# Performance work log

Hardware: AMD Instinct MI355X
Metric: run time of the kernel (lower is better)

The kernel has to match this reference:

```python
import jax, jax.numpy as jnp
import numpy as np

DIM = 64
B_GRAPHS = 16
N_NODES = 4096
N_EDGES = 16384
SLOPE = 0.01  # PyTorch leaky_relu default negative slope


def lrelu(x):
    return jnp.where(x >= 0, x, SLOPE * x)


def setup_inputs() -> dict:
    key = jax.random.key(0)
    ks = jax.random.split(key, 16)
    d = DIM

    def rn(k, shape, scale=0.05):
        return jax.random.normal(k, shape, dtype=jnp.float32) * scale

    def z(*s):
        return jnp.zeros(s, jnp.float32)

    return {
        "x": jax.random.normal(ks[0], (N_NODES, 3), dtype=jnp.float32),
        "edge_attr": jax.random.normal(ks[1], (N_EDGES, 4), dtype=jnp.float32),
        "edge_index": jax.random.randint(ks[2], (2, N_EDGES), 0, N_NODES),
        "batch": jnp.sort(jax.random.randint(ks[3], (N_NODES,), 0, B_GRAPHS)),
        # lin0
        "W0": rn(ks[4], (3, d)), "b0": z(d),
        # edge MLP: Linear(4,d) -> LeakyReLU -> Linear(d, d*d)
        "We1": rn(ks[5], (4, d)), "be1": z(d),
        "We2": rn(ks[6], (d, d * d), 0.01), "be2": z(d * d),
        # NNConv root weight + bias
        "root": rn(ks[7], (d, d)), "conv_b": z(d),
        # GRU(d, d)  (PyTorch layout: [3d, in] / [3d, hid], gate order r,z,n)
        "Wih": rn(ks[8], (3 * d, d)), "Whh": rn(ks[9], (3 * d, d)),
        "bih": z(3 * d), "bhh": z(3 * d),
        # Set2Set LSTM(2d, d)  (gate order i,f,g,o)
        "lWih": rn(ks[10], (4 * d, 2 * d)), "lWhh": rn(ks[11], (4 * d, d)),
        "lbih": z(4 * d), "lbhh": z(4 * d),
        # lin_out: Linear(2d, 2)
        "Wout": rn(ks[12], (2 * d, 2)), "bout": z(2),
    }


def _forward(x, edge_attr, W0, b0, We1, be1, We2, be2, root, conv_b,
             Wih, Whh, bih, bhh, lWih, lWhh, lbih, lbhh, Wout, bout,
             edge_index, batch):
    d = DIM
    N = x.shape[0]
    E = edge_attr.shape[0]
    src, dst = edge_index[0], edge_index[1]  # messages flow src(j) -> dst(i)

    out = lrelu(x @ W0 + b0)  # [N, d]
    h = out                    # GRU hidden state (h = out.unsqueeze(0))

    # Edge-conditioned weights: constant across the 6 iterations, compute once.
    he = lrelu(edge_attr @ We1 + be1)          # [E, d]
    W_e = (he @ We2 + be2).reshape(E, d, d)    # [E, d, d]
    deg = jax.ops.segment_sum(jnp.ones((E,), jnp.float32), dst, num_segments=N)
    inv_deg = (1.0 / jnp.maximum(deg, 1.0))[:, None]  # mean aggr, clamp like PyG

    for _ in range(6):
        # NNConv: gather x_j, per-edge matmul, scatter-mean, plus root term
        msg = jnp.einsum('ed,edf->ef', out[src], W_e)            # [E, d]
        agg = jax.ops.segment_sum(msg, dst, num_segments=N) * inv_deg
        m = lrelu(agg + out @ root + conv_b)                     # [N, d]
        # GRU cell (single step, PyTorch gate order r, z, n)
        gi = m @ Wih.T + bih
        gh = h @ Whh.T + bhh
        i_r, i_z, i_n = jnp.split(gi, 3, axis=-1)
        h_r, h_z, h_n = jnp.split(gh, 3, axis=-1)
        r = jax.nn.sigmoid(i_r + h_r)
        zg = jax.nn.sigmoid(i_z + h_z)
        n = jnp.tanh(i_n + r * h_n)
        h = (1.0 - zg) * n + zg * h
        out = h

    # Set2Set pooling, processing_steps = 1
    Bg = B_GRAPHS
    q_star = jnp.zeros((Bg, 2 * d), jnp.float32)
    hl = jnp.zeros((Bg, d), jnp.float32)
    cl = jnp.zeros((Bg, d), jnp.float32)
    gates = q_star @ lWih.T + lbih + hl @ lWhh.T + lbhh
    gi_, gf_, gg_, go_ = jnp.split(gates, 4, axis=-1)
    cl = jax.nn.sigmoid(gf_) * cl + jax.nn.sigmoid(gi_) * jnp.tanh(gg_)
    q = jax.nn.sigmoid(go_) * jnp.tanh(cl)         # [Bg, d]
    e = jnp.sum(out * q[batch], axis=-1)           # [N]
    emax = jax.ops.segment_max(e, batch, num_segments=Bg)
    a = jnp.exp(e - emax[batch])
    asum = jax.ops.segment_sum(a, batch, num_segments=Bg)
    a = a / asum[batch]                            # per-graph softmax attention
    rpool = jax.ops.segment_sum(a[:, None] * out, batch, num_segments=Bg)
    q_star = jnp.concatenate([q, rpool], axis=-1)  # [Bg, 2d]

    return q_star @ Wout + bout                    # [Bg, 2]


def reference(x, edge_attr, edge_index, batch, W0, b0, We1, be1, We2, be2,
              root, conv_b, Wih, Whh, bih, bhh, lWih, lWhh, lbih, lbhh,
              Wout, bout):
    return _forward(x, edge_attr, W0, b0, We1, be1, We2, be2, root, conv_b,
                    Wih, Whh, bih, bhh, lWih, lWhh, lbih, lbhh, Wout, bout,
                    edge_index, batch)
```

## Files before the change

kernel.cpp:

```cpp
#include <hip/hip_runtime.h>
#include <cstddef>

#define NE 16384
#define NN 4096
#define BG 16
#define NT 16
#define ACH 16

__device__ __forceinline__ float lrelu(float v){ return v >= 0.f ? v : 0.01f*v; }
__device__ __forceinline__ float sigm(float v){ return 1.f/(1.f + expf(-v)); }

__global__ __launch_bounds__(256) void setup_kernel(
    const float* __restrict__ x, const float* __restrict__ ea,
    const int* __restrict__ ei,
    const float* __restrict__ W0, const float* __restrict__ b0,
    const float* __restrict__ We1, const float* __restrict__ be1,
    const float* __restrict__ Wih, const float* __restrict__ Whh,
    float* __restrict__ WihT, float* __restrict__ WhhT,
    float* __restrict__ h, float* __restrict__ he,
    int* __restrict__ deg, int* __restrict__ cnt)
{
    int t = blockIdx.x*256 + threadIdx.x;
    {
        int e = t >> 6, f = t & 63;
        float v = be1[f];
        #pragma unroll
        for (int d = 0; d < 4; ++d) v += ea[e*4+d]*We1[d*64+f];
        he[t] = lrelu(v);
    }
    if (t < NN*64) {
        int n = t >> 6, f = t & 63;
        float v = b0[f];
        #pragma unroll
        for (int d = 0; d < 3; ++d) v += x[n*3+d]*W0[d*64+f];
        h[t] = lrelu(v);
    }
    if (t < 12288) {
        int k = t / 192, g = t - k*192;
        WihT[t] = Wih[g*64 + k];
        WhhT[t] = Whh[g*64 + k];
    }
    if (t < NE) {
        atomicAdd(&deg[ei[NE + t]], 1);
        atomicAdd(&cnt[ei[t]], 1);
    }
}

__global__ __launch_bounds__(256) void scan_kernel(const int* __restrict__ cnt,
                                                   int* __restrict__ offs)
{
    __shared__ int ps[256];
    int t = threadIdx.x;
    int base = t*16;
    int loc[16];
    int s = 0;
    #pragma unroll
    for (int i = 0; i < 16; ++i) { loc[i] = s; s += cnt[base+i]; }
    ps[t] = s; __syncthreads();
    for (int off = 1; off < 256; off <<= 1) {
        int v = 0;
        if (t >= off) v = ps[t-off];
        __syncthreads();
        if (t >= off) ps[t] += v;
        __syncthreads();
    }
    int pre = (t == 0) ? 0 : ps[t-1];
    #pragma unroll
    for (int i = 0; i < 16; ++i) offs[base+i] = pre + loc[i];
    if (t == 255) offs[NN] = pre + s;
}

__global__ __launch_bounds__(256) void scatter_kernel(
    const int* __restrict__ ei, const int* __restrict__ offs,
    int* __restrict__ cnt,
    int* __restrict__ srcs, int* __restrict__ dsts, int* __restrict__ perm)
{
    int e = blockIdx.x*256 + threadIdx.x;
    if (e >= NE) return;
    int s = ei[e], d = ei[NE + e];
    int old = atomicSub(&cnt[s], 1);
    int pos = offs[s] + old - 1;
    srcs[pos] = s; dsts[pos] = d; perm[pos] = e;
}

__global__ __launch_bounds__(256) void reorder_kernel(
    const float* __restrict__ he, const int* __restrict__ perm,
    float* __restrict__ he_srt)
{
    int t = blockIdx.x*256 + threadIdx.x;
    he_srt[t] = he[(size_t)perm[t>>6]*64 + (t & 63)];
}

__global__ __launch_bounds__(256) void inv_range_kernel(
    const int* __restrict__ deg, const int* __restrict__ batch,
    float* __restrict__ inv_deg, int* __restrict__ gstart, int* __restrict__ gend)
{
    int n = blockIdx.x*256 + threadIdx.x;
    if (n >= NN) return;
    inv_deg[n] = 1.f / fmaxf((float)deg[n], 1.f);
    int b  = batch[n];
    int bp = (n == 0)    ? -1 : batch[n-1];
    int bn = (n == NN-1) ? BG : batch[n+1];
    for (int g = bp+1; g <= b; ++g) gstart[g] = n;
    for (int g = b;   g <  bn; ++g) gend[g]   = n+1;
    if (n == 0)    for (int g = 0;   g < b;  ++g) gend[g]   = 0;
    if (n == NN-1) for (int g = b+1; g < BG; ++g) gstart[g] = NN;
}

__global__ __launch_bounds__(1024) void conv_kernel(
    const float* __restrict__ h, const float* __restrict__ We2,
    const float* __restrict__ be2, const float* __restrict__ he_srt,
    const int* __restrict__ offs, const int* __restrict__ srcs,
    const int* __restrict__ dsts, float* __restrict__ agg)
{
    __shared__ float hsT[64][NT];
    __shared__ float Tb [NT][64];
    __shared__ float Tc [ACH][NT][64];
    int t  = threadIdx.x;
    int n0 = blockIdx.x * NT;

    {
        int n = t >> 6, i = t & 63;
        hsT[i][n] = h[(size_t)(n0+n)*64 + i];
    }
    __syncthreads();
    {
        int n = t >> 6, f = t & 63;
        float acc = 0.f;
        #pragma unroll 8
        for (int i = 0; i < 64; ++i) acc += hsT[i][n] * be2[i*64+f];
        Tb[n][f] = acc;
    }

    int ebase = offs[n0];
    int ecnt  = offs[n0+NT] - ebase;
    int eend  = ebase + ecnt;
    int slot  = t >> 4;
    int f4    = (t & 15) * 4;
    int e0 = ebase + slot, e1 = ebase + slot + 64;
    int nl0 = -1, dt0 = 0, nl1 = -1, dt1 = 0;
    if (slot < ecnt)       { nl0 = srcs[e0] - n0; dt0 = dsts[e0]; }
    if (slot + 64 < ecnt)  { nl1 = srcs[e1] - n0; dt1 = dsts[e1]; }
    float4 m0 = {0,0,0,0}, m1 = {0,0,0,0};

    int aT = t >> 6;
    int fT = (t & 15) * 4;
    int nT = ((t >> 4) & 3) * 4;

    for (int c = 0; c < 4; ++c) {
        const float* Wp = We2 + ((size_t)(c*ACH + aT))*4096 + fT;
        float4 A0 = {0,0,0,0}, A1 = {0,0,0,0}, A2 = {0,0,0,0}, A3 = {0,0,0,0};
        #pragma unroll 8
        for (int i = 0; i < 64; ++i) {
            float4 w  = *(const float4*)(Wp + (size_t)i*64);
            float4 hv = *(const float4*)&hsT[i][nT];
            A0.x += hv.x*w.x; A0.y += hv.x*w.y; A0.z += hv.x*w.z; A0.w += hv.x*w.w;
            A1.x += hv.y*w.x; A1.y += hv.y*w.y; A1.z += hv.y*w.z; A1.w += hv.y*w.w;
            A2.x += hv.z*w.x; A2.y += hv.z*w.y; A2.z += hv.z*w.z; A2.w += hv.z*w.w;
            A3.x += hv.w*w.x; A3.y += hv.w*w.y; A3.z += hv.w*w.z; A3.w += hv.w*w.w;
        }
        __syncthreads();
        *(float4*)&Tc[aT][nT+0][fT] = A0;
        *(float4*)&Tc[aT][nT+1][fT] = A1;
        *(float4*)&Tc[aT][nT+2][fT] = A2;
        *(float4*)&Tc[aT][nT+3][fT] = A3;
        __syncthreads();

        if (nl0 >= 0) {
            const float* hep = he_srt + (size_t)e0*64 + c*ACH;
            #pragma unroll
            for (int a = 0; a < ACH; ++a) {
                float hv = hep[a];
                float4 tv = *(const float4*)&Tc[a][nl0][f4];
                m0.x += hv*tv.x; m0.y += hv*tv.y; m0.z += hv*tv.z; m0.w += hv*tv.w;
            }
        }
        if (nl1 >= 0) {
            const float* hep = he_srt + (size_t)e1*64 + c*ACH;
            #pragma unroll
            for (int a = 0; a < ACH; ++a) {
                float hv = hep[a];
                float4 tv = *(const float4*)&Tc[a][nl1][f4];
                m1.x += hv*tv.x; m1.y += hv*tv.y; m1.z += hv*tv.z; m1.w += hv*tv.w;
            }
        }
        for (int e = ebase + 128 + slot; e < eend; e += 64) {
            int nl = srcs[e] - n0, dt = dsts[e];
            const float* hep = he_srt + (size_t)e*64 + c*ACH;
            float4 pm = {0,0,0,0};
            #pragma unroll
            for (int a = 0; a < ACH; ++a) {
                float hv = hep[a];
                float4 tv = *(const float4*)&Tc[a][nl][f4];
                pm.x += hv*tv.x; pm.y += hv*tv.y; pm.z += hv*tv.z; pm.w += hv*tv.w;
            }
            if (c == 0) {
                float4 b = *(const float4*)&Tb[nl][f4];
                pm.x += b.x; pm.y += b.y; pm.z += b.z; pm.w += b.w;
            }
            float* ap = agg + (size_t)dt*64 + f4;
            atomicAdd(ap+0, pm.x); atomicAdd(ap+1, pm.y);
            atomicAdd(ap+2, pm.z); atomicAdd(ap+3, pm.w);
        }
    }

    if (nl0 >= 0) {
        float4 b = *(const float4*)&Tb[nl0][f4];
        float* ap = agg + (size_t)dt0*64 + f4;
        atomicAdd(ap+0, m0.x+b.x); atomicAdd(ap+1, m0.y+b.y);
        atomicAdd(ap+2, m0.z+b.z); atomicAdd(ap+3, m0.w+b.w);
    }
    if (nl1 >= 0) {
        float4 b = *(const float4*)&Tb[nl1][f4];
        float* ap = agg + (size_t)dt1*64 + f4;
        atomicAdd(ap+0, m1.x+b.x); atomicAdd(ap+1, m1.y+b.y);
        atomicAdd(ap+2, m1.z+b.z); atomicAdd(ap+3, m1.w+b.w);
    }
}

__global__ __launch_bounds__(512) void node_kernel(
    const float* __restrict__ WihT, const float* __restrict__ WhhT,
    const float* __restrict__ root, const float* __restrict__ conv_b,
    const float* __restrict__ inv_deg, const float* __restrict__ bih,
    const float* __restrict__ bhh, float* __restrict__ h,
    float* __restrict__ agg)
{
    __shared__ float WT[64][392];
    __shared__ float hT[64][34];
    __shared__ float mT[64][34];
    int t  = threadIdx.x;
    int n0 = blockIdx.x * 32;

    #pragma unroll
    for (int i = 0; i < 24; ++i) {
        int idx = t + i*512;
        int k = idx / 192, c = idx - k*192;
        WT[k][c]       = WihT[idx];
        WT[k][196 + c] = WhhT[idx];
    }
    #pragma unroll
    for (int i = 0; i < 4; ++i) {
        int idx = t + i*512;
        int n = idx >> 6, d = idx & 63;
        hT[d][n] = h[(size_t)(n0+n)*64 + d];
    }
    __syncthreads();
    #pragma unroll
    for (int i = 0; i < 4; ++i) {
        int idx = t + i*512;
        int n = idx >> 6, d = idx & 63;
        int gn = n0 + n;
        float v = agg[(size_t)gn*64 + d]*inv_deg[gn] + conv_b[d];
        agg[(size_t)gn*64 + d] = 0.f;
        #pragma unroll 8
        for (int k = 0; k < 64; ++k) v += hT[k][n]*root[k*64 + d];
        mT[d][n] = lrelu(v);
    }
    __syncthreads();

    int tx = t & 31, ty = t >> 5;
    float ai[2][2][3] = {{{0.f}}};
    float ah[2][2][3] = {{{0.f}}};
    #pragma unroll 8
    for (int k = 0; k < 64; ++k) {
        float2 am = *(float2*)&mT[k][ty*2];
        float2 av = *(float2*)&hT[k][ty*2];
        #pragma unroll
        for (int g = 0; g < 3; ++g) {
            float2 bi = *(float2*)&WT[k][g*64 + tx*2];
            float2 bh = *(float2*)&WT[k][196 + g*64 + tx*2];
            ai[0][0][g] += am.x*bi.x; ai[0][1][g] += am.x*bi.y;
            ai[1][0][g] += am.y*bi.x; ai[1][1][g] += am.y*bi.y;
            ah[0][0][g] += av.x*bh.x; ah[0][1][g] += av.x*bh.y;
            ah[1][0][g] += av.y*bh.x; ah[1][1][g] += av.y*bh.y;
        }
    }
    #pragma unroll
    for (int i = 0; i < 2; ++i) {
        int n = ty*2 + i, gn = n0 + n;
        #pragma unroll
        for (int j = 0; j < 2; ++j) {
            int g = tx*2 + j;
            float r  = sigm(ai[i][j][0] + bih[g]      + ah[i][j][0] + bhh[g]);
            float z  = sigm(ai[i][j][1] + bih[64+g]   + ah[i][j][1] + bhh[64+g]);
            float nn = tanhf(ai[i][j][2] + bih[128+g] + r*(ah[i][j][2] + bhh[128+g]));
            float ho = hT[g][n];
            h[(size_t)gn*64 + g] = (1.f - z)*nn + z*ho;
        }
    }
}

__device__ __forceinline__ float q_val(const float* lbih, const float* lbhh, int g)
{
    float gi = lbih[g]     + lbhh[g];
    float gg = lbih[128+g] + lbhh[128+g];
    float go = lbih[192+g] + lbhh[192+g];
    return sigm(go)*tanhf(sigm(gi)*tanhf(gg));
}

__global__ __launch_bounds__(256) void e_kernel(
    const float* __restrict__ h, const float* __restrict__ lbih,
    const float* __restrict__ lbhh, float* __restrict__ e)
{
    __shared__ float qs[64];
    int t = threadIdx.x;
    if (t < 64) qs[t] = q_val(lbih, lbhh, t);
    __syncthreads();
    int w = t >> 6, f = t & 63;
    int n = blockIdx.x*4 + w;
    float p = h[(size_t)n*64 + f]*qs[f];
    #pragma unroll
    for (int off = 32; off; off >>= 1) p += __shfl_xor(p, off);
    if (f == 0) e[n] = p;
}

__global__ __launch_bounds__(1024) void pool_kernel(
    const float* __restrict__ h, float* __restrict__ e,
    const int* __restrict__ gstart, const int* __restrict__ gend,
    const float* __restrict__ lbih, const float* __restrict__ lbhh,
    const float* __restrict__ Wout, const float* __restrict__ bout,
    float* __restrict__ out)
{
    __shared__ float red[1024];
    __shared__ float rp[64];
    __shared__ float sval;
    int g = blockIdx.x, t = threadIdx.x;
    int s = gstart[g], en = gend[g];

    float mx = -1e30f;
    for (int n = s+t; n < en; n += 1024) mx = fmaxf(mx, e[n]);
    red[t] = mx; __syncthreads();
    for (int st = 512; st; st >>= 1) { if (t < st) red[t] = fmaxf(red[t], red[t+st]); __syncthreads(); }
    if (t == 0) sval = red[0];
    __syncthreads();
    float lmx = sval;
    __syncthreads();

    float sm = 0.f;
    for (int n = s+t; n < en; n += 1024) { float a = expf(e[n]-lmx); e[n] = a; sm += a; }
    red[t] = sm; __syncthreads();
    for (int st = 512; st; st >>= 1) { if (t < st) red[t] += red[t+st]; __syncthreads(); }
    if (t == 0) sval = (red[0] > 0.f) ? 1.f/red[0] : 0.f;
    __syncthreads();
    float inv_asum = sval;
    __syncthreads();

    int w = t >> 6, f = t & 63;
    float racc = 0.f;
    for (int n = s+w; n < en; n += 16) racc += e[n]*h[(size_t)n*64 + f];
    red[t] = racc; __syncthreads();
    if (w == 0) {
        float a = 0.f;
        #pragma unroll
        for (int i = 0; i < 16; ++i) a += red[i*64 + f];
        rp[f] = a*inv_asum;
    }
    __syncthreads();

    if (t < 64) {
        float qv = q_val(lbih, lbhh, t);
        float p0 = qv*Wout[t*2]   + rp[t]*Wout[(64+t)*2];
        float p1 = qv*Wout[t*2+1] + rp[t]*Wout[(64+t)*2+1];
        #pragma unroll
        for (int off = 32; off; off >>= 1) { p0 += __shfl_xor(p0, off); p1 += __shfl_xor(p1, off); }
        if (t == 0) { out[g*2] = p0 + bout[0]; out[g*2+1] = p1 + bout[1]; }
    }
}

extern "C" void kernel_launch(void* const* d_in, const int* in_sizes, int n_in,
                              void* d_out, int out_size, void* d_ws, size_t ws_size,
                              hipStream_t stream)
{
    const float* x      = (const float*)d_in[0];
    const float* ea     = (const float*)d_in[1];
    const int*   ei     = (const int*)  d_in[2];
    const int*   batch  = (const int*)  d_in[3];
    const float* W0     = (const float*)d_in[4];
    const float* b0     = (const float*)d_in[5];
    const float* We1    = (const float*)d_in[6];
    const float* be1    = (const float*)d_in[7];
    const float* We2    = (const float*)d_in[8];
    const float* be2    = (const float*)d_in[9];
    const float* root   = (const float*)d_in[10];
    const float* conv_b = (const float*)d_in[11];
    const float* Wih    = (const float*)d_in[12];
    const float* Whh    = (const float*)d_in[13];
    const float* bih    = (const float*)d_in[14];
    const float* bhh    = (const float*)d_in[15];
    const float* lbih   = (const float*)d_in[18];
    const float* lbhh   = (const float*)d_in[19];
    const float* Wout   = (const float*)d_in[20];
    const float* bout   = (const float*)d_in[21];
    float* out = (float*)d_out;

    float* W = (float*)d_ws;
    size_t off = 0;
    float* h       = W + off; off += (size_t)NN*64;
    float* he      = W + off; off += (size_t)NE*64;
    float* he_srt  = W + off; off += (size_t)NE*64;
    float* agg     = W + off; off += (size_t)NN*64;
    float* WihT    = W + off; off += 12288;
    float* WhhT    = W + off; off += 12288;
    float* inv_deg = W + off; off += NN;
    float* e       = W + off; off += NN;
    int*   deg     = (int*)(W + off); off += NN;
    int*   cnt     = (int*)(W + off); off += NN;
    int*   offs    = (int*)(W + off); off += NN+1;
    int*   srcs    = (int*)(W + off); off += NE;
    int*   dsts    = (int*)(W + off); off += NE;
    int*   perm    = (int*)(W + off); off += NE;
    int*   gstart  = (int*)(W + off); off += BG;
    int*   gend    = (int*)(W + off); off += BG;

    hipMemsetAsync(deg, 0, 2*NN*sizeof(int), stream);
    hipMemsetAsync(agg, 0, (size_t)NN*64*sizeof(float), stream);
    setup_kernel<<<4096, 256, 0, stream>>>(x, ea, ei, W0, b0, We1, be1, Wih, Whh,
                                           WihT, WhhT, h, he, deg, cnt);
    scan_kernel<<<1, 256, 0, stream>>>(cnt, offs);
    scatter_kernel<<<64, 256, 0, stream>>>(ei, offs, cnt, srcs, dsts, perm);
    reorder_kernel<<<4096, 256, 0, stream>>>(he, perm, he_srt);
    inv_range_kernel<<<16, 256, 0, stream>>>(deg, batch, inv_deg, gstart, gend);

    for (int it = 0; it < 6; ++it) {
        conv_kernel<<<NN/NT, 1024, 0, stream>>>(h, We2, be2, he_srt,
                                                offs, srcs, dsts, agg);
        node_kernel<<<NN/32, 512, 0, stream>>>(WihT, WhhT, root, conv_b,
                                               inv_deg, bih, bhh, h, agg);
    }

    e_kernel<<<NN/4, 256, 0, stream>>>(h, lbih, lbhh, e);
    pool_kernel<<<BG, 1024, 0, stream>>>(h, e, gstart, gend, lbih, lbhh, Wout, bout, out);
}
```

Baseline: 573.1 us.

## Split conv kernel over edge-feature halves and simplify GRU node kernel

The conv kernel grid gains a second dimension, so each block handles half of the 64 edge-feature columns. This doubles the number of blocks and halves the per-block serial chunk loop. Edge features for the first 128 edges are staged in shared memory and read with float4 vector loads. The node kernel is rewritten to give each thread one (node, gate) pair over 8 nodes per block, reading an interleaved, padded transposed GRU weight layout from global memory instead of staging the full weight matrices in LDS. The cost is twice as many atomic adds into agg and more redundant global weight reads per block.

```diff
diff --git a/kernel.cpp b/kernel.cpp
--- a/kernel.cpp
+++ b/kernel.cpp
@@ -16,7 +16,7 @@
     const float* __restrict__ W0, const float* __restrict__ b0,
     const float* __restrict__ We1, const float* __restrict__ be1,
     const float* __restrict__ Wih, const float* __restrict__ Whh,
-    float* __restrict__ WihT, float* __restrict__ WhhT,
+    float* __restrict__ W8T,
     float* __restrict__ h, float* __restrict__ he,
     int* __restrict__ deg, int* __restrict__ cnt)
 {
@@ -35,10 +35,12 @@
         for (int d = 0; d < 3; ++d) v += x[n*3+d]*W0[d*64+f];
         h[t] = lrelu(v);
     }
-    if (t < 12288) {
-        int k = t / 192, g = t - k*192;
-        WihT[t] = Wih[g*64 + k];
-        WhhT[t] = Whh[g*64 + k];
+    if (t < 32768) {
+        int k = t >> 9, g = (t >> 3) & 63, j = t & 7;
+        float v = 0.f;
+        if (j < 3)      v = Wih[(j*64+g)*64 + k];
+        else if (j < 6) v = Whh[((j-3)*64+g)*64 + k];
+        W8T[t] = v;
     }
     if (t < NE) {
         atomicAdd(&deg[ei[NE + t]], 1);
@@ -107,7 +109,7 @@
     if (n == NN-1) for (int g = b+1; g < BG; ++g) gstart[g] = NN;
 }
 
-__global__ __launch_bounds__(1024) void conv_kernel(
+__global__ __launch_bounds__(1024, 8) void conv_kernel(
     const float* __restrict__ h, const float* __restrict__ We2,
     const float* __restrict__ be2, const float* __restrict__ he_srt,
     const int* __restrict__ offs, const int* __restrict__ srcs,
@@ -116,15 +118,14 @@
     __shared__ float hsT[64][NT];
     __shared__ float Tb [NT][64];
     __shared__ float Tc [ACH][NT][64];
+    __shared__ float he_s[128][16];
     int t  = threadIdx.x;
     int n0 = blockIdx.x * NT;
-
-    {
-        int n = t >> 6, i = t & 63;
-        hsT[i][n] = h[(size_t)(n0+n)*64 + i];
-    }
-    __syncthreads();
-    {
+    int a0 = blockIdx.y * 32;
+
+    { int n = t >> 6, i = t & 63; hsT[i][n] = h[(size_t)(n0+n)*64 + i]; }
+    __syncthreads();
+    if (blockIdx.y == 0) {
         int n = t >> 6, f = t & 63;
         float acc = 0.f;
         #pragma unroll 8
@@ -137,18 +138,20 @@
     int eend  = ebase + ecnt;
     int slot  = t >> 4;
     int f4    = (t & 15) * 4;
-    int e0 = ebase + slot, e1 = ebase + slot + 64;
+    int e0 = ebase + slot, e1 = ebase + 64 + slot;
     int nl0 = -1, dt0 = 0, nl1 = -1, dt1 = 0;
-    if (slot < ecnt)       { nl0 = srcs[e0] - n0; dt0 = dsts[e0]; }
-    if (slot + 64 < ecnt)  { nl1 = srcs[e1] - n0; dt1 = dsts[e1]; }
+    if (slot < ecnt)      { nl0 = srcs[e0] - n0; dt0 = dsts[e0]; }
+    if (64 + slot < ecnt) { nl1 = srcs[e1] - n0; dt1 = dsts[e1]; }
     float4 m0 = {0,0,0,0}, m1 = {0,0,0,0};
 
     int aT = t >> 6;
     int fT = (t & 15) * 4;
     int nT = ((t >> 4) & 3) * 4;
 
-    for (int c = 0; c < 4; ++c) {
-        const float* Wp = We2 + ((size_t)(c*ACH + aT))*4096 + fT;
+    #pragma unroll
+    for (int c = 0; c < 2; ++c) {
+        int ac = a0 + c*ACH;
+        const float* Wp = We2 + (size_t)(ac + aT)*4096 + fT;
         float4 A0 = {0,0,0,0}, A1 = {0,0,0,0}, A2 = {0,0,0,0}, A3 = {0,0,0,0};
         #pragma unroll 8
         for (int i = 0; i < 64; ++i) {
@@ -164,37 +167,60 @@
         *(float4*)&Tc[aT][nT+1][fT] = A1;
         *(float4*)&Tc[aT][nT+2][fT] = A2;
         *(float4*)&Tc[aT][nT+3][fT] = A3;
+        {
+            int le = t >> 3, a2 = (t & 7)*2;
+            int e = ebase + le;
+            if (e < NE)
+                *(float2*)&he_s[le][a2] =
+                    *(const float2*)&he_srt[(size_t)e*64 + ac + a2];
+        }
         __syncthreads();
 
         if (nl0 >= 0) {
-            const float* hep = he_srt + (size_t)e0*64 + c*ACH;
             #pragma unroll
-            for (int a = 0; a < ACH; ++a) {
-                float hv = hep[a];
-                float4 tv = *(const float4*)&Tc[a][nl0][f4];
-                m0.x += hv*tv.x; m0.y += hv*tv.y; m0.z += hv*tv.z; m0.w += hv*tv.w;
+            for (int a4 = 0; a4 < 4; ++a4) {
+                float4 hv = *(const float4*)&he_s[slot][a4*4];
+                float4 t0 = *(const float4*)&Tc[a4*4+0][nl0][f4];
+                float4 t1 = *(const float4*)&Tc[a4*4+1][nl0][f4];
+                float4 t2 = *(const float4*)&Tc[a4*4+2][nl0][f4];
+                float4 t3 = *(const float4*)&Tc[a4*4+3][nl0][f4];
+                m0.x += hv.x*t0.x + hv.y*t1.x + hv.z*t2.x + hv.w*t3.x;
+                m0.y += hv.x*t0.y + hv.y*t1.y + hv.z*t2.y + hv.w*t3.y;
+                m0.z += hv.x*t0.z + hv.y*t1.z + hv.z*t2.z + hv.w*t3.z;
+                m0.w += hv.x*t0.w + hv.y*t1.w + hv.z*t2.w + hv.w*t3.w;
             }
         }
         if (nl1 >= 0) {
-            const float* hep = he_srt + (size_t)e1*64 + c*ACH;
             #pragma unroll
-            for (int a = 0; a < ACH; ++a) {
-                float hv = hep[a];
-                float4 tv = *(const float4*)&Tc[a][nl1][f4];
-                m1.x += hv*tv.x; m1.y += hv*tv.y; m1.z += hv*tv.z; m1.w += hv*tv.w;
+            for (int a4 = 0; a4 < 4; ++a4) {
+                float4 hv = *(const float4*)&he_s[64+slot][a4*4];
+                float4 t0 = *(const float4*)&Tc[a4*4+0][nl1][f4];
+                float4 t1 = *(const float4*)&Tc[a4*4+1][nl1][f4];
+                float4 t2 = *(const float4*)&Tc[a4*4+2][nl1][f4];
+                float4 t3 = *(const float4*)&Tc[a4*4+3][nl1][f4];
+                m1.x += hv.x*t0.x + hv.y*t1.x + hv.z*t2.x + hv.w*t3.x;
+                m1.y += hv.x*t0.y + hv.y*t1.y + hv.z*t2.y + hv.w*t3.y;
+                m1.z += hv.x*t0.z + hv.y*t1.z + hv.z*t2.z + hv.w*t3.z;
+                m1.w += hv.x*t0.w + hv.y*t1.w + hv.z*t2.w + hv.w*t3.w;
             }
         }
         for (int e = ebase + 128 + slot; e < eend; e += 64) {
             int nl = srcs[e] - n0, dt = dsts[e];
-            const float* hep = he_srt + (size_t)e*64 + c*ACH;
+            const float* hep = he_srt + (size_t)e*64 + ac;
             float4 pm = {0,0,0,0};
             #pragma unroll
-            for (int a = 0; a < ACH; ++a) {
-                float hv = hep[a];
-                float4 tv = *(const float4*)&Tc[a][nl][f4];
-                pm.x += hv*tv.x; pm.y += hv*tv.y; pm.z += hv*tv.z; pm.w += hv*tv.w;
+            for (int a4 = 0; a4 < 4; ++a4) {
+                float4 hv = *(const float4*)(hep + a4*4);
+                float4 t0 = *(const float4*)&Tc[a4*4+0][nl][f4];
+                float4 t1 = *(const float4*)&Tc[a4*4+1][nl][f4];
+                float4 t2 = *(const float4*)&Tc[a4*4+2][nl][f4];
+                float4 t3 = *(const float4*)&Tc[a4*4+3][nl][f4];
+                pm.x += hv.x*t0.x + hv.y*t1.x + hv.z*t2.x + hv.w*t3.x;
+                pm.y += hv.x*t0.y + hv.y*t1.y + hv.z*t2.y + hv.w*t3.y;
+                pm.z += hv.x*t0.z + hv.y*t1.z + hv.z*t2.z + hv.w*t3.z;
+                pm.w += hv.x*t0.w + hv.y*t1.w + hv.z*t2.w + hv.w*t3.w;
             }
-            if (c == 0) {
+            if (blockIdx.y == 0 && c == 0) {
                 float4 b = *(const float4*)&Tb[nl][f4];
                 pm.x += b.x; pm.y += b.y; pm.z += b.z; pm.w += b.w;
             }
@@ -204,14 +230,15 @@
         }
     }
 
+    bool addb = (blockIdx.y == 0);
     if (nl0 >= 0) {
-        float4 b = *(const float4*)&Tb[nl0][f4];
+        float4 b = addb ? *(const float4*)&Tb[nl0][f4] : make_float4(0,0,0,0);
         float* ap = agg + (size_t)dt0*64 + f4;
         atomicAdd(ap+0, m0.x+b.x); atomicAdd(ap+1, m0.y+b.y);
         atomicAdd(ap+2, m0.z+b.z); atomicAdd(ap+3, m0.w+b.w);
     }
     if (nl1 >= 0) {
-        float4 b = *(const float4*)&Tb[nl1][f4];
+        float4 b = addb ? *(const float4*)&Tb[nl1][f4] : make_float4(0,0,0,0);
         float* ap = agg + (size_t)dt1*64 + f4;
         atomicAdd(ap+0, m1.x+b.x); atomicAdd(ap+1, m1.y+b.y);
         atomicAdd(ap+2, m1.z+b.z); atomicAdd(ap+3, m1.w+b.w);
@@ -219,75 +246,41 @@
 }
 
 __global__ __launch_bounds__(512) void node_kernel(
-    const float* __restrict__ WihT, const float* __restrict__ WhhT,
-    const float* __restrict__ root, const float* __restrict__ conv_b,
-    const float* __restrict__ inv_deg, const float* __restrict__ bih,
-    const float* __restrict__ bhh, float* __restrict__ h,
-    float* __restrict__ agg)
-{
-    __shared__ float WT[64][392];
-    __shared__ float hT[64][34];
-    __shared__ float mT[64][34];
-    int t  = threadIdx.x;
-    int n0 = blockIdx.x * 32;
-
-    #pragma unroll
-    for (int i = 0; i < 24; ++i) {
-        int idx = t + i*512;
-        int k = idx / 192, c = idx - k*192;
-        WT[k][c]       = WihT[idx];
-        WT[k][196 + c] = WhhT[idx];
-    }
-    #pragma unroll
-    for (int i = 0; i < 4; ++i) {
-        int idx = t + i*512;
-        int n = idx >> 6, d = idx & 63;
-        hT[d][n] = h[(size_t)(n0+n)*64 + d];
-    }
-    __syncthreads();
-    #pragma unroll
-    for (int i = 0; i < 4; ++i) {
-        int idx = t + i*512;
-        int n = idx >> 6, d = idx & 63;
-        int gn = n0 + n;
-        float v = agg[(size_t)gn*64 + d]*inv_deg[gn] + conv_b[d];
-        agg[(size_t)gn*64 + d] = 0.f;
+    const float* __restrict__ W8T, const float* __restrict__ root,
+    const float* __restrict__ conv_b, const float* __restrict__ inv_deg,
+    const float* __restrict__ bih, const float* __restrict__ bhh,
+    float* __restrict__ h, float* __restrict__ agg)
+{
+    __shared__ float hs[8][64];
+    __shared__ float ms[8][64];
+    int t = threadIdx.x;
+    int n = t >> 6, g = t & 63;
+    int gn = blockIdx.x*8 + n;
+    hs[n][g] = h[(size_t)gn*64 + g];
+    __syncthreads();
+    {
+        float v = agg[(size_t)gn*64 + g]*inv_deg[gn] + conv_b[g];
+        agg[(size_t)gn*64 + g] = 0.f;
         #pragma unroll 8
-        for (int k = 0; k < 64; ++k) v += hT[k][n]*root[k*64 + d];
-        mT[d][n] = lrelu(v);
-    }
-    __syncthreads();
-
-    int tx = t & 31, ty = t >> 5;
-    float ai[2][2][3] = {{{0.f}}};
-    float ah[2][2][3] = {{{0.f}}};
+        for (int k = 0; k < 64; ++k) v += hs[n][k]*root[k*64 + g];
+        ms[n][g] = lrelu(v);
+    }
+    __syncthreads();
+
+    float ir=0.f, iz=0.f, in_=0.f, hr=0.f, hz=0.f, hn=0.f;
+    const float* Wp = W8T + (size_t)g*8;
     #pragma unroll 8
     for (int k = 0; k < 64; ++k) {
-        float2 am = *(float2*)&mT[k][ty*2];
-        float2 av = *(float2*)&hT[k][ty*2];
-        #pragma unroll
-        for (int g = 0; g < 3; ++g) {
-            float2 bi = *(float2*)&WT[k][g*64 + tx*2];
-            float2 bh = *(float2*)&WT[k][196 + g*64 + tx*2];
-            ai[0][0][g] += am.x*bi.x; ai[0][1][g] += am.x*bi.y;
-            ai[1][0][g] += am.y*bi.x; ai[1][1][g] += am.y*bi.y;
-            ah[0][0][g] += av.x*bh.x; ah[0][1][g] += av.x*bh.y;
-            ah[1][0][g] += av.y*bh.x; ah[1][1][g] += av.y*bh.y;
-        }
-    }
-    #pragma unroll
-    for (int i = 0; i < 2; ++i) {
-        int n = ty*2 + i, gn = n0 + n;
-        #pragma unroll
-        for (int j = 0; j < 2; ++j) {
-            int g = tx*2 + j;
-            float r  = sigm(ai[i][j][0] + bih[g]      + ah[i][j][0] + bhh[g]);
-            float z  = sigm(ai[i][j][1] + bih[64+g]   + ah[i][j][1] + bhh[64+g]);
-            float nn = tanhf(ai[i][j][2] + bih[128+g] + r*(ah[i][j][2] + bhh[128+g]));
-            float ho = hT[g][n];
-            h[(size_t)gn*64 + g] = (1.f - z)*nn + z*ho;
-        }
-    }
+        float am = ms[n][k], ah = hs[n][k];
+        float4 w0 = *(const float4*)(Wp + (size_t)k*512);
+        float4 w1 = *(const float4*)(Wp + (size_t)k*512 + 4);
+        ir  += am*w0.x; iz += am*w0.y; in_ += am*w0.z;
+        hr  += ah*w0.w; hz += ah*w1.x; hn  += ah*w1.y;
+    }
+    float r  = sigm(ir + bih[g]      + hr + bhh[g]);
+    float z  = sigm(iz + bih[64+g]   + hz + bhh[64+g]);
+    float nn = tanhf(in_ + bih[128+g] + r*(hn + bhh[128+g]));
+    h[(size_t)gn*64 + g] = (1.f - z)*nn + z*hs[n][g];
 }
 
 __device__ __forceinline__ float q_val(const float* lbih, const float* lbhh, int g)
@@ -399,8 +392,7 @@
     float* he      = W + off; off += (size_t)NE*64;
     float* he_srt  = W + off; off += (size_t)NE*64;
     float* agg     = W + off; off += (size_t)NN*64;
-    float* WihT    = W + off; off += 12288;
-    float* WhhT    = W + off; off += 12288;
+    float* W8T     = W + off; off += 32768;
     float* inv_deg = W + off; off += NN;
     float* e       = W + off; off += NN;
     int*   deg     = (int*)(W + off); off += NN;
@@ -415,17 +407,17 @@
     hipMemsetAsync(deg, 0, 2*NN*sizeof(int), stream);
     hipMemsetAsync(agg, 0, (size_t)NN*64*sizeof(float), stream);
     setup_kernel<<<4096, 256, 0, stream>>>(x, ea, ei, W0, b0, We1, be1, Wih, Whh,
-                                           WihT, WhhT, h, he, deg, cnt);
+                                           W8T, h, he, deg, cnt);
     scan_kernel<<<1, 256, 0, stream>>>(cnt, offs);
     scatter_kernel<<<64, 256, 0, stream>>>(ei, offs, cnt, srcs, dsts, perm);
     reorder_kernel<<<4096, 256, 0, stream>>>(he, perm, he_srt);
     inv_range_kernel<<<16, 256, 0, stream>>>(deg, batch, inv_deg, gstart, gend);
 
     for (int it = 0; it < 6; ++it) {
-        conv_kernel<<<NN/NT, 1024, 0, stream>>>(h, We2, be2, he_srt,
-                                                offs, srcs, dsts, agg);
-        node_kernel<<<NN/32, 512, 0, stream>>>(WihT, WhhT, root, conv_b,
-                                               inv_deg, bih, bhh, h, agg);
+        conv_kernel<<<dim3(NN/NT, 2), 1024, 0, stream>>>(h, We2, be2, he_srt,
+                                                         offs, srcs, dsts, agg);
+        node_kernel<<<NN/8, 512, 0, stream>>>(W8T, root, conv_b,
+                                              inv_deg, bih, bhh, h, agg);
     }
 
     e_kernel<<<NN/4, 256, 0, stream>>>(h, lbih, lbhh, e);
```

Result: slower. 711.1 us (+24.1%).
